# Kernel optimization log

Measured on AMD Instinct MI355X. Metric: run time of the kernel, lower is better.

## Reference

```python
import jax, jax.numpy as jnp
import numpy as np

BS, SEQ_LEN, N_NODES = 16, 12, 512
D, H, L, K = 256, 8, 2, 16
DFF = 4 * D
DH = D // H


def setup_inputs() -> dict:
    key = jax.random.key(0)
    ks = jax.random.split(key, 12)
    p = lambda i, shape: jax.random.normal(ks[i], shape, dtype=jnp.float32) * 0.02
    return dict(
        x_c=jax.random.normal(ks[0], (BS, SEQ_LEN, N_NODES), dtype=jnp.float32),
        A=jax.random.uniform(ks[1], (N_NODES, N_NODES), dtype=jnp.float32),
        W_src_emb=p(2, (SEQ_LEN, D)),
        W_tgt_emb=p(3, (SEQ_LEN, D)),
        enc_attn=p(4, (L, 4, D, D)),
        enc_ffn1=p(5, (L, D, DFF)),
        enc_ffn2=p(6, (L, DFF, D)),
        dec_self=p(7, (L, 4, D, D)),
        dec_cross=p(8, (L, 4, D, D)),
        dec_ffn1=p(9, (L, D, DFF)),
        dec_ffn2=p(10, (L, DFF, D)),
        W_gen=p(11, (D, SEQ_LEN)),
    )


def _ln(x):
    m = jnp.mean(x, axis=-1, keepdims=True)
    v = jnp.var(x, axis=-1, keepdims=True)
    return (x - m) * jax.lax.rsqrt(v + 1e-6)


def _mha(xq, xkv, W):
    # xq: [b, n, q, D], xkv: [b, n, s, D], W: [4, D, D]
    q = (xq @ W[0]).reshape(xq.shape[:-1] + (H, DH))
    k = (xkv @ W[1]).reshape(xkv.shape[:-1] + (H, DH))
    v = (xkv @ W[2]).reshape(xkv.shape[:-1] + (H, DH))
    sc = jnp.einsum('bnqhe,bnkhe->bnhqk', q, k) / np.float32(np.sqrt(DH))
    a = jax.nn.softmax(sc, axis=-1)
    o = jnp.einsum('bnhqk,bnkhe->bnqhe', a, v)
    o = o.reshape(o.shape[:-2] + (D,))
    return o @ W[3]


def _pe(length):
    pos = jnp.arange(length, dtype=jnp.float32)[:, None]
    div = jnp.exp(jnp.arange(0, D, 2, dtype=jnp.float32) * (-np.log(10000.0) / D))
    pe = jnp.zeros((length, D), dtype=jnp.float32)
    pe = pe.at[:, 0::2].set(jnp.sin(pos * div)).at[:, 1::2].set(jnp.cos(pos * div))
    return pe


def reference(x_c, A, W_src_emb, W_tgt_emb, enc_attn, enc_ffn1, enc_ffn2,
              dec_self, dec_cross, dec_ffn1, dec_ffn2, W_gen):
    # x_c: [bs, seq_len, N] -> x: [bs, N, seq_len]
    x = jnp.transpose(x_c, (0, 2, 1))
    # top-k neighbors per node (descending by A)
    index = jnp.argsort(-A, axis=-1)[:, :K]            # [N, K]
    sx = x[:, index]                                   # [bs, N, K, seq_len]  (the gather)
    tgt_in = x[:, :, None, :]                          # [bs, N, 1, seq_len]

    scale = np.float32(np.sqrt(D))
    src = sx @ W_src_emb * scale + _pe(K)              # [bs, N, K, D]
    tgt = tgt_in @ W_tgt_emb * scale + _pe(1)          # [bs, N, 1, D]

    # encoder (pre-norm residual sublayers, annotated-transformer style)
    for l in range(L):
        y = _ln(src)
        src = src + _mha(y, y, enc_attn[l])
        y = _ln(src)
        src = src + jax.nn.relu(y @ enc_ffn1[l]) @ enc_ffn2[l]
    memory = _ln(src)

    # decoder
    for l in range(L):
        y = _ln(tgt)
        tgt = tgt + _mha(y, y, dec_self[l])
        y = _ln(tgt)
        tgt = tgt + _mha(y, memory, dec_cross[l])
        y = _ln(tgt)
        tgt = tgt + jax.nn.relu(y @ dec_ffn1[l]) @ dec_ffn2[l]
    out = _ln(tgt) @ W_gen                             # [bs, N, 1, seq_len]
    return out[:, :, 0, :]                             # squeeze(-2): [bs, N, seq_len]
```

## Files before the change

kernel.cpp:

```cpp
#include <hip/hip_runtime.h>

typedef unsigned short u16;
typedef unsigned int u32;
typedef __attribute__((ext_vector_type(8))) short short8;
typedef __attribute__((ext_vector_type(4))) float f32x4;

__device__ __forceinline__ float bf2f(unsigned v){ union{unsigned u; float f;} c; c.u = v<<16; return c.f; }
__device__ __forceinline__ u16 f2bf(float f){
  union{float f; unsigned u;} c; c.f=f;
  unsigned u = c.u;
  u += 0x7fffu + ((u>>16)&1u);
  return (u16)(u>>16);
}
__device__ __forceinline__ float bfLO(u32 x){ union{u32 u; float f;} c; c.u = x<<16;        return c.f; }
__device__ __forceinline__ float bfHI(u32 x){ union{u32 u; float f;} c; c.u = x&0xffff0000u; return c.f; }
__device__ __forceinline__ u32 pack2(float a, float b){ return (u32)f2bf(a) | ((u32)f2bf(b)<<16); }

__device__ __forceinline__ float hsum32(float v){
  #pragma unroll
  for(int off=16; off>0; off>>=1) v += __shfl_xor(v, off);
  return v;
}

#define GLDS(g, l) __builtin_amdgcn_global_load_lds( \
    (const __attribute__((address_space(1))) void*)(g), \
    (__attribute__((address_space(3))) void*)(l), 16, 0, 0)

__global__ void topk_kernel(const float* __restrict__ A, int* __restrict__ idx){
  __shared__ float vals[512];
  const int n = blockIdx.x, t = threadIdx.x;
  for(int i=t;i<512;i+=64) vals[i] = A[n*512+i];
  __syncthreads();
  for(int kk=0;kk<16;kk++){
    float bv = -1e30f; int bi = 1<<30;
    for(int i=t;i<512;i+=64){
      float v = vals[i];
      if(v > bv){ bv=v; bi=i; }
    }
    #pragma unroll
    for(int off=32; off>0; off>>=1){
      float ov = __shfl_down(bv, off);
      int   oi = __shfl_down(bi, off);
      if(ov > bv || (ov==bv && oi<bi)){ bv=ov; bi=oi; }
    }
    bi = __shfl(bi, 0);
    if(t==0){ idx[n*16+kk] = bi; vals[bi] = -1e30f; }
    __syncthreads();
  }
}

__global__ __launch_bounds__(256)
void tcvt_kernel(const float* __restrict__ src, u16* __restrict__ dst, int R, int C){
  __shared__ float t[32][33];
  const int m = blockIdx.z;
  src += (size_t)m*R*C; dst += (size_t)m*R*C;
  const int c0 = blockIdx.x*32, r0 = blockIdx.y*32;
  const int tx = threadIdx.x, ty = threadIdx.y;
  #pragma unroll
  for(int i=0;i<4;i++) t[ty*4+i][tx] = src[(size_t)(r0+ty*4+i)*C + c0+tx];
  __syncthreads();
  #pragma unroll
  for(int i=0;i<4;i++) dst[(size_t)(c0+ty*4+i)*R + r0+tx] = f2bf(t[tx][ty*4+i]);
}

__global__ void cvt_kernel(const float* __restrict__ in, u16* __restrict__ out, int n4){
  int i = blockIdx.x*256 + threadIdx.x;
  if(i>=n4) return;
  float4 v = ((const float4*)in)[i];
  ushort4 o; o.x=f2bf(v.x); o.y=f2bf(v.y); o.z=f2bf(v.z); o.w=f2bf(v.w);
  ((ushort4*)out)[i] = o;
}

__global__ void embed_kernel(const float* __restrict__ x_c, const int* __restrict__ idx,
                             const float* __restrict__ Wsrc, const float* __restrict__ Wtgt,
                             u16* __restrict__ S, u16* __restrict__ TGT, int g0){
  __shared__ float xs[16][12];
  __shared__ float xt[12];
  const int gl = blockIdx.x, g = gl + g0, b = g>>9, n = g&511, d = threadIdx.x;
  if(d < 192){ int kk=d/12, t=d-kk*12; xs[kk][t] = x_c[(b*12+t)*512 + idx[n*16+kk]]; }
  else if(d < 204){ int t=d-192; xt[t] = x_c[(b*12+t)*512 + n]; }
  __syncthreads();
  float wsr[12], wtg[12];
  #pragma unroll
  for(int t=0;t<12;t++){ wsr[t]=Wsrc[t*256+d]; wtg[t]=Wtgt[t*256+d]; }
  const float freq = expf(-(float)(d & ~1) * (9.210340371976184f/256.0f));
  const bool odd = d & 1;
  for(int kk=0;kk<16;kk++){
    float a=0;
    #pragma unroll
    for(int t=0;t<12;t++) a = fmaf(xs[kk][t], wsr[t], a);
    float pe = odd ? cosf(freq*(float)kk) : sinf(freq*(float)kk);
    S[(size_t)(gl*16+kk)*256 + d] = f2bf(a*16.0f + pe);
  }
  float a=0;
  #pragma unroll
  for(int t=0;t<12;t++) a = fmaf(xt[t], wtg[t], a);
  TGT[(size_t)gl*256 + d] = f2bf(a*16.0f + (odd?1.0f:0.0f));
}

__global__ __launch_bounds__(256) void ln_kernel(const u16* __restrict__ X, u16* __restrict__ Y){
  const int tid = threadIdx.x;
  const int lh = tid & 31;
  const size_t row = (size_t)blockIdx.x*8 + (tid>>5);
  const size_t base = row*256 + (size_t)lh*8;
  uint4 u = *(const uint4*)(X + base);
  float x[8];
  x[0]=bfLO(u.x); x[1]=bfHI(u.x); x[2]=bfLO(u.y); x[3]=bfHI(u.y);
  x[4]=bfLO(u.z); x[5]=bfHI(u.z); x[6]=bfLO(u.w); x[7]=bfHI(u.w);
  float s=0;
  #pragma unroll
  for(int i=0;i<8;i++) s += x[i];
  float mean = hsum32(s) * (1.0f/256.0f);
  float v=0;
  #pragma unroll
  for(int i=0;i<8;i++){ x[i]-=mean; v += x[i]*x[i]; }
  float sc = rsqrtf(hsum32(v)*(1.0f/256.0f) + 1e-6f);
  uint4 o;
  o.x = pack2(x[0]*sc, x[1]*sc); o.y = pack2(x[2]*sc, x[3]*sc);
  o.z = pack2(x[4]*sc, x[5]*sc); o.w = pack2(x[6]*sc, x[7]*sc);
  *(uint4*)(Y + base) = o;
}

template<int MODE>
__global__ __launch_bounds__(256)
void gemm_mfma(const u16* __restrict__ A, const u16* __restrict__ Bt, u16* __restrict__ C,
               int M, int N, int K)
{
  __shared__ u16 As[128*32];
  __shared__ u16 Bs[128*32];
  const int tid = threadIdx.x;
  const int w = tid>>6, l = tid&63;
  const int quad = l>>4, col16 = l&15;
  const int wr = (w>>1)*64, wc = (w&1)*64;
  const size_t m0 = (size_t)blockIdx.x*128;
  const size_t n0 = (size_t)blockIdx.y*128;

  const int sr = l>>2, sc = (l&3)*8;
  const int ca = w*2, cb = w*2+1;
  const u16* aG0 = A  + (m0 + ca*16 + sr)*K + sc;
  const u16* aG1 = A  + (m0 + cb*16 + sr)*K + sc;
  const u16* bG0 = Bt + (n0 + ca*16 + sr)*K + sc;
  const u16* bG1 = Bt + (n0 + cb*16 + sr)*K + sc;
  u16* aL0 = &As[ca*512];
  u16* aL1 = &As[cb*512];
  u16* bL0 = &Bs[ca*512];
  u16* bL1 = &Bs[cb*512];

  f32x4 acc[4][4];
  #pragma unroll
  for(int i=0;i<4;i++)
    #pragma unroll
    for(int j=0;j<4;j++) acc[i][j] = (f32x4){0.f,0.f,0.f,0.f};

  for(int k0=0;k0<K;k0+=32){
    GLDS(aG0 + k0, aL0);
    GLDS(aG1 + k0, aL1);
    GLDS(bG0 + k0, bL0);
    GLDS(bG1 + k0, bL1);
    __syncthreads();
    short8 af[4], bf[4];
    #pragma unroll
    for(int i=0;i<4;i++) af[i] = *(const short8*)&As[(wr + i*16 + col16)*32 + quad*8];
    #pragma unroll
    for(int j=0;j<4;j++) bf[j] = *(const short8*)&Bs[(wc + j*16 + col16)*32 + quad*8];
    #pragma unroll
    for(int i=0;i<4;i++)
      #pragma unroll
      for(int j=0;j<4;j++)
        acc[i][j] = __builtin_amdgcn_mfma_f32_16x16x32_bf16(af[i], bf[j], acc[i][j], 0,0,0);
    __syncthreads();
  }

  #pragma unroll
  for(int i=0;i<4;i++){
    #pragma unroll
    for(int r=0;r<4;r++){
      const size_t row = m0 + wr + i*16 + quad*4 + r;
      u16* cp = C + row*(size_t)N + n0 + wc + col16;
      #pragma unroll
      for(int j=0;j<4;j++){
        float v = acc[i][j][r];
        if(MODE==2) v += bf2f(cp[j*16]);
        if(MODE==1) v = fmaxf(v, 0.f);
        cp[j*16] = f2bf(v);
      }
    }
  }
}

__global__ __launch_bounds__(256)
void attn_enc_kernel(const u16* __restrict__ QKV, u16* __restrict__ O){
  __shared__ u16 sh[2][12672];
  const int tid = threadIdx.x;
  const int half = tid>>7, th = tid&127;
  const size_t g = (size_t)blockIdx.x*2 + half;
  const size_t grow = g*16;
  u16* sb = sh[half];
  #pragma unroll
  for(int it=0; it<12; it++){
    int e = (th + 128*it)*8;
    int r = e/768, c = e - r*768;
    int t = c>>8, cc = c&255;
    *(uint4*)&sb[t*4224 + r*264 + cc] = *(const uint4*)&QKV[(grow+r)*768 + c];
  }
  __syncthreads();
  const int h = th>>4, q = th&15;
  const int ho = h*32;
  float qv[32];
  #pragma unroll
  for(int e2=0;e2<16;e2++){
    u32 x = *(const u32*)&sb[q*264 + ho + e2*2];
    qv[2*e2]=bfLO(x); qv[2*e2+1]=bfHI(x);
  }
  float sc[16];
  #pragma unroll
  for(int kk=0;kk<16;kk++){
    const u16* kr = &sb[4224 + kk*264 + ho];
    float s=0;
    #pragma unroll
    for(int e2=0;e2<16;e2++){
      u32 x = *(const u32*)&kr[e2*2];
      s = fmaf(qv[2*e2], bfLO(x), s);
      s = fmaf(qv[2*e2+1], bfHI(x), s);
    }
    sc[kk] = s*0.17677669529663687f;
  }
  float m=sc[0];
  #pragma unroll
  for(int kk=1;kk<16;kk++) m=fmaxf(m,sc[kk]);
  float sum=0;
  #pragma unroll
  for(int kk=0;kk<16;kk++){ sc[kk]=expf(sc[kk]-m); sum+=sc[kk]; }
  float inv=1.0f/sum;
  float ov[32];
  #pragma unroll
  for(int e=0;e<32;e++) ov[e]=0.f;
  #pragma unroll
  for(int kk=0;kk<16;kk++){
    float p = sc[kk]*inv;
    const u16* vr = &sb[8448 + kk*264 + ho];
    #pragma unroll
    for(int e2=0;e2<16;e2++){
      u32 x = *(const u32*)&vr[e2*2];
      ov[2*e2]   = fmaf(p, bfLO(x), ov[2*e2]);
      ov[2*e2+1] = fmaf(p, bfHI(x), ov[2*e2+1]);
    }
  }
  u16* op = O + (grow+q)*256 + ho;
  #pragma unroll
  for(int b=0;b<8;b++){
    ushort4 t4; t4.x=f2bf(ov[4*b]); t4.y=f2bf(ov[4*b+1]); t4.z=f2bf(ov[4*b+2]); t4.w=f2bf(ov[4*b+3]);
    *(ushort4*)&op[b*4] = t4;
  }
}

__global__ __launch_bounds__(256)
void attn_cross_kernel(const u16* __restrict__ Qc, const u16* __restrict__ KV,
                       u16* __restrict__ Oc, int loff){
  __shared__ float qs[256];
  __shared__ float ks[16*264], vs[16*264];
  __shared__ float aw[128];
  const int t = threadIdx.x;
  const size_t g = blockIdx.x;
  qs[t] = bf2f(Qc[g*256+t]);
  for(int i=t;i<4096;i+=256){
    int r=i>>8, c=i&255;
    int li = r*264 + ((c>>5)*33) + (c&31);
    const u16* p = KV + (g*16+r)*1024 + loff + c;
    ks[li]=bf2f(p[0]); vs[li]=bf2f(p[256]);
  }
  __syncthreads();
  if(t<128){
    int h=t>>4, kk=t&15;
    float s=0;
    #pragma unroll
    for(int e=0;e<32;e++) s = fmaf(qs[h*32+e], ks[kk*264+h*33+e], s);
    aw[h*16+kk] = s*0.17677669529663687f;
  }
  __syncthreads();
  if(t<8){
    float m=-1e30f;
    for(int kk=0;kk<16;kk++) m=fmaxf(m, aw[t*16+kk]);
    float sum=0;
    for(int kk=0;kk<16;kk++){ float e=expf(aw[t*16+kk]-m); aw[t*16+kk]=e; sum+=e; }
    float inv=1.0f/sum;
    for(int kk=0;kk<16;kk++) aw[t*16+kk]*=inv;
  }
  __syncthreads();
  {
    int h=t>>5, e=t&31;
    float o=0;
    #pragma unroll
    for(int kk=0;kk<16;kk++) o = fmaf(aw[h*16+kk], vs[kk*264+h*33+e], o);
    Oc[g*256+t] = f2bf(o);
  }
}

__global__ __launch_bounds__(64)
void final_kernel(const u16* __restrict__ T, const float* __restrict__ Wg, float* __restrict__ out, int g0){
  __shared__ float y[256];
  const int lane = threadIdx.x;
  const size_t gl = blockIdx.x;
  ushort4 u = *(const ushort4*)(T + gl*256 + (size_t)lane*4);
  float x0=bf2f(u.x), x1=bf2f(u.y), x2=bf2f(u.z), x3=bf2f(u.w);
  float s4 = x0+x1+x2+x3;
  #pragma unroll
  for(int off=32; off>0; off>>=1) s4 += __shfl_xor(s4, off);
  float mean = s4*(1.0f/256.0f);
  float d0=x0-mean,d1=x1-mean,d2=x2-mean,d3=x3-mean;
  float v4 = d0*d0+d1*d1+d2*d2+d3*d3;
  #pragma unroll
  for(int off=32; off>0; off>>=1) v4 += __shfl_xor(v4, off);
  float sc = rsqrtf(v4*(1.0f/256.0f)+1e-6f);
  y[lane*4+0]=d0*sc; y[lane*4+1]=d1*sc; y[lane*4+2]=d2*sc; y[lane*4+3]=d3*sc;
  __syncthreads();
  if(lane<12){
    float s=0;
    for(int d=0;d<256;d++) s = fmaf(y[d], Wg[d*12+lane], s);
    out[(g0+gl)*12+lane]=s;
  }
}

extern "C" void kernel_launch(void* const* d_in, const int* in_sizes, int n_in,
                              void* d_out, int out_size, void* d_ws, size_t ws_size,
                              hipStream_t stream)
{
  (void)in_sizes; (void)n_in; (void)out_size;
  const float* x_c  = (const float*)d_in[0];
  const float* A    = (const float*)d_in[1];
  const float* Wsrc = (const float*)d_in[2];
  const float* Wtgt = (const float*)d_in[3];
  const float* wsrc_f[7] = {(const float*)d_in[4],(const float*)d_in[5],(const float*)d_in[6],
                            (const float*)d_in[7],(const float*)d_in[8],(const float*)d_in[9],
                            (const float*)d_in[10]};
  const float* W_gen = (const float*)d_in[11];
  float* out = (float*)d_out;

  auto align256 = [](size_t b)->size_t{ return (b + 255) & ~(size_t)255; };
  auto need_bytes = [&](int GC)->size_t{
    size_t b = 0;
    b += align256(512*16*4);
    for(int i=0;i<7;i++) b += align256((size_t)524288*2);
    b += align256((size_t)4*65536*2);
    b += align256((size_t)2*65536*2)*2;
    b += align256((size_t)GC*16*256*2)*2;
    b += align256((size_t)GC*16*1024*2);
    b += align256((size_t)GC*256*2)*4;
    b += align256((size_t)GC*1024*2);
    return b;
  };
  int GC = 8192;
  while(GC > 128 && need_bytes(GC) > ws_size) GC >>= 1;

  char* ws = (char*)d_ws;
  size_t off = 0;
  auto alloc = [&](size_t bytes)->char*{
    char* p = ws + off;
    off += (bytes + 255) & ~(size_t)255;
    return p;
  };
  int* idx = (int*)alloc(512*16*4);
  u16* wt[7];
  for(int i=0;i<7;i++) wt[i] = (u16*)alloc((size_t)524288*2);
  u16* wKV      = (u16*)alloc((size_t)4*65536*2);
  u16* wv_plain = (u16*)alloc((size_t)2*65536*2);
  u16* wVO      = (u16*)alloc((size_t)2*65536*2);
  u16* cS  = (u16*)alloc((size_t)GC*16*256*2);
  u16* cY  = (u16*)alloc((size_t)GC*16*256*2);
  u16* big = (u16*)alloc((size_t)GC*16*1024*2);
  u16* tgt = (u16*)alloc((size_t)GC*256*2);
  u16* tY  = (u16*)alloc((size_t)GC*256*2);
  u16* tA  = (u16*)alloc((size_t)GC*256*2);
  u16* tO  = (u16*)alloc((size_t)GC*256*2);
  u16* tT  = (u16*)alloc((size_t)GC*1024*2);

  u16* wQKV = big;
  u16* Tc   = big;
  u16* KVc  = big;

  {
    dim3 blk(32,8);
    tcvt_kernel<<<dim3( 256/32, 256/32, 8), blk, 0, stream>>>(wsrc_f[0], wt[0], 256, 256);
    tcvt_kernel<<<dim3(1024/32, 256/32, 2), blk, 0, stream>>>(wsrc_f[1], wt[1], 256,1024);
    tcvt_kernel<<<dim3( 256/32,1024/32, 2), blk, 0, stream>>>(wsrc_f[2], wt[2],1024, 256);
    tcvt_kernel<<<dim3( 256/32, 256/32, 8), blk, 0, stream>>>(wsrc_f[3], wt[3], 256, 256);
    tcvt_kernel<<<dim3( 256/32, 256/32, 8), blk, 0, stream>>>(wsrc_f[4], wt[4], 256, 256);
    tcvt_kernel<<<dim3(1024/32, 256/32, 2), blk, 0, stream>>>(wsrc_f[5], wt[5], 256,1024);
    tcvt_kernel<<<dim3( 256/32,1024/32, 2), blk, 0, stream>>>(wsrc_f[6], wt[6],1024, 256);
  }
  topk_kernel<<<512,64,0,stream>>>(A, idx);

  hipMemcpyAsync(wKV+0*65536, wt[4]+1*65536, 65536*2, hipMemcpyDeviceToDevice, stream);
  hipMemcpyAsync(wKV+1*65536, wt[4]+2*65536, 65536*2, hipMemcpyDeviceToDevice, stream);
  hipMemcpyAsync(wKV+2*65536, wt[4]+5*65536, 65536*2, hipMemcpyDeviceToDevice, stream);
  hipMemcpyAsync(wKV+3*65536, wt[4]+6*65536, 65536*2, hipMemcpyDeviceToDevice, stream);

  for(int l=0;l<2;l++){
    cvt_kernel<<<64,256,0,stream>>>(wsrc_f[3]+(size_t)(l*4+2)*65536, wv_plain+(size_t)l*65536, 16384);
    gemm_mfma<0><<<dim3(2,2),256,0,stream>>>(wt[3]+(size_t)(l*4+3)*65536, wv_plain+(size_t)l*65536,
                                             wVO+(size_t)l*65536, 256,256,256);
  }

  auto gemm = [&](const u16* Am, const u16* Bm, u16* Cm, int M_, int N_, int K_, int mode){
    dim3 grid(M_/128, N_/128);
    if(mode==1)      gemm_mfma<1><<<grid,256,0,stream>>>(Am,Bm,Cm,M_,N_,K_);
    else if(mode==2) gemm_mfma<2><<<grid,256,0,stream>>>(Am,Bm,Cm,M_,N_,K_);
    else             gemm_mfma<0><<<grid,256,0,stream>>>(Am,Bm,Cm,M_,N_,K_);
  };

  const int Mr = GC*16;
  const int Md = GC;

  for(int g0=0; g0<8192; g0+=GC){
    embed_kernel<<<GC,256,0,stream>>>(x_c, idx, Wsrc, Wtgt, cS, tgt, g0);

    for(int l=0;l<2;l++){
      const u16* Wat = wt[0] + (size_t)l*4*65536;
      ln_kernel<<<Mr/8,256,0,stream>>>(cS, cY);
      gemm(cY, Wat,           wQKV, Mr, 768, 256, 0);
      attn_enc_kernel<<<GC/2,256,0,stream>>>(wQKV, cY);
      gemm(cY, Wat+3*65536,   cS,   Mr, 256, 256, 2);
      ln_kernel<<<Mr/8,256,0,stream>>>(cS, cY);
      gemm(cY, wt[1]+(size_t)l*262144, Tc, Mr,1024, 256, 1);
      gemm(Tc, wt[2]+(size_t)l*262144, cS, Mr, 256,1024, 2);
    }
    ln_kernel<<<Mr/8,256,0,stream>>>(cS, cY);
    gemm(cY, wKV, KVc, Mr, 1024, 256, 0);

    for(int l=0;l<2;l++){
      const u16* Wdc = wt[4] + (size_t)l*4*65536;
      ln_kernel<<<Md/8,256,0,stream>>>(tgt, tY);
      gemm(tY, wVO+(size_t)l*65536, tgt, Md, 256, 256, 2);
      ln_kernel<<<Md/8,256,0,stream>>>(tgt, tY);
      gemm(tY, Wdc,          tA,  Md, 256, 256, 0);
      attn_cross_kernel<<<GC,256,0,stream>>>(tA, KVc, tO, l*512);
      gemm(tO, Wdc+3*65536,  tgt, Md, 256, 256, 2);
      ln_kernel<<<Md/8,256,0,stream>>>(tgt, tY);
      gemm(tY, wt[5]+(size_t)l*262144, tT,  Md,1024, 256, 1);
      gemm(tT, wt[6]+(size_t)l*262144, tgt, Md, 256,1024, 2);
    }

    final_kernel<<<GC,64,0,stream>>>(tgt, W_gen, out, g0);
  }
}
```

Baseline: 1.902 ms.

## Fuse LayerNorm into residual GEMM epilogues and embedding kernel

Adds a gemm_addln kernel where each block covers a full 256-wide row, does the residual add, computes the row mean and variance across waves through shared memory, and writes both the residual stream and its normalized copy. The embedding kernel also emits the normalized source and target, and final_kernel now reads the already-normalized target. Together these remove every standalone ln_kernel launch and the extra read and write of activations it caused. In exchange the fused GEMM uses a 128x256 tile with a larger accumulator array, so register pressure rises and fewer blocks launch, and variance is now computed as E[x²]-mean², which is less numerically robust.

```diff
diff --git a/kernel.cpp b/kernel.cpp
--- a/kernel.cpp
+++ b/kernel.cpp
@@ -15,12 +15,6 @@
 __device__ __forceinline__ float bfLO(u32 x){ union{u32 u; float f;} c; c.u = x<<16;        return c.f; }
 __device__ __forceinline__ float bfHI(u32 x){ union{u32 u; float f;} c; c.u = x&0xffff0000u; return c.f; }
 __device__ __forceinline__ u32 pack2(float a, float b){ return (u32)f2bf(a) | ((u32)f2bf(b)<<16); }
-
-__device__ __forceinline__ float hsum32(float v){
-  #pragma unroll
-  for(int off=16; off>0; off>>=1) v += __shfl_xor(v, off);
-  return v;
-}
 
 #define GLDS(g, l) __builtin_amdgcn_global_load_lds( \
     (const __attribute__((address_space(1))) void*)(g), \
@@ -71,12 +65,19 @@
   ((ushort4*)out)[i] = o;
 }
 
-__global__ void embed_kernel(const float* __restrict__ x_c, const int* __restrict__ idx,
-                             const float* __restrict__ Wsrc, const float* __restrict__ Wtgt,
-                             u16* __restrict__ S, u16* __restrict__ TGT, int g0){
+__global__ __launch_bounds__(256)
+void embed_kernel(const float* __restrict__ x_c, const int* __restrict__ idx,
+                  const float* __restrict__ Wsrc, const float* __restrict__ Wtgt,
+                  u16* __restrict__ S, u16* __restrict__ SY,
+                  u16* __restrict__ TGT, u16* __restrict__ TGTY, int g0){
   __shared__ float xs[16][12];
   __shared__ float xt[12];
+  __shared__ float sm[16][260];
+  __shared__ float mv[16][2];
+  __shared__ float wpart[4][2];
+  __shared__ float tmv[2];
   const int gl = blockIdx.x, g = gl + g0, b = g>>9, n = g&511, d = threadIdx.x;
+  const int w = d>>6, lane = d&63;
   if(d < 192){ int kk=d/12, t=d-kk*12; xs[kk][t] = x_c[(b*12+t)*512 + idx[n*16+kk]]; }
   else if(d < 204){ int t=d-192; xt[t] = x_c[(b*12+t)*512 + n]; }
   __syncthreads();
@@ -85,40 +86,57 @@
   for(int t=0;t<12;t++){ wsr[t]=Wsrc[t*256+d]; wtg[t]=Wtgt[t*256+d]; }
   const float freq = expf(-(float)(d & ~1) * (9.210340371976184f/256.0f));
   const bool odd = d & 1;
+  float xv[16];
+  #pragma unroll
   for(int kk=0;kk<16;kk++){
     float a=0;
     #pragma unroll
     for(int t=0;t<12;t++) a = fmaf(xs[kk][t], wsr[t], a);
     float pe = odd ? cosf(freq*(float)kk) : sinf(freq*(float)kk);
-    S[(size_t)(gl*16+kk)*256 + d] = f2bf(a*16.0f + pe);
-  }
-  float a=0;
-  #pragma unroll
-  for(int t=0;t<12;t++) a = fmaf(xt[t], wtg[t], a);
-  TGT[(size_t)gl*256 + d] = f2bf(a*16.0f + (odd?1.0f:0.0f));
-}
-
-__global__ __launch_bounds__(256) void ln_kernel(const u16* __restrict__ X, u16* __restrict__ Y){
-  const int tid = threadIdx.x;
-  const int lh = tid & 31;
-  const size_t row = (size_t)blockIdx.x*8 + (tid>>5);
-  const size_t base = row*256 + (size_t)lh*8;
-  uint4 u = *(const uint4*)(X + base);
-  float x[8];
-  x[0]=bfLO(u.x); x[1]=bfHI(u.x); x[2]=bfLO(u.y); x[3]=bfHI(u.y);
-  x[4]=bfLO(u.z); x[5]=bfHI(u.z); x[6]=bfLO(u.w); x[7]=bfHI(u.w);
-  float s=0;
-  #pragma unroll
-  for(int i=0;i<8;i++) s += x[i];
-  float mean = hsum32(s) * (1.0f/256.0f);
-  float v=0;
-  #pragma unroll
-  for(int i=0;i<8;i++){ x[i]-=mean; v += x[i]*x[i]; }
-  float sc = rsqrtf(hsum32(v)*(1.0f/256.0f) + 1e-6f);
-  uint4 o;
-  o.x = pack2(x[0]*sc, x[1]*sc); o.y = pack2(x[2]*sc, x[3]*sc);
-  o.z = pack2(x[4]*sc, x[5]*sc); o.w = pack2(x[6]*sc, x[7]*sc);
-  *(uint4*)(Y + base) = o;
+    xv[kk] = a*16.0f + pe;
+    S[(size_t)(gl*16+kk)*256 + d] = f2bf(xv[kk]);
+    sm[kk][d] = xv[kk];
+  }
+  float tv;
+  {
+    float a=0;
+    #pragma unroll
+    for(int t=0;t<12;t++) a = fmaf(xt[t], wtg[t], a);
+    tv = a*16.0f + (odd?1.0f:0.0f);
+    TGT[(size_t)gl*256 + d] = f2bf(tv);
+  }
+  {
+    float s2=tv, q2=tv*tv;
+    #pragma unroll
+    for(int off=32; off>0; off>>=1){ s2+=__shfl_xor(s2,off); q2+=__shfl_xor(q2,off); }
+    if(lane==0){ wpart[w][0]=s2; wpart[w][1]=q2; }
+  }
+  __syncthreads();
+  {
+    const int kk=d>>4, part=d&15;
+    float s=0,q=0;
+    #pragma unroll
+    for(int t=0;t<16;t++){ float v=sm[kk][part*16+t]; s+=v; q+=v*v; }
+    #pragma unroll
+    for(int off=1; off<16; off<<=1){ s+=__shfl_xor(s,off); q+=__shfl_xor(q,off); }
+    if(part==0){
+      float mean=s*(1.0f/256.0f);
+      float var=q*(1.0f/256.0f)-mean*mean;
+      mv[kk][0]=mean; mv[kk][1]=rsqrtf(var+1e-6f);
+    }
+    if(d==0){
+      float ts=wpart[0][0]+wpart[1][0]+wpart[2][0]+wpart[3][0];
+      float tq=wpart[0][1]+wpart[1][1]+wpart[2][1]+wpart[3][1];
+      float mean=ts*(1.0f/256.0f);
+      float var=tq*(1.0f/256.0f)-mean*mean;
+      tmv[0]=mean; tmv[1]=rsqrtf(var+1e-6f);
+    }
+  }
+  __syncthreads();
+  #pragma unroll
+  for(int kk=0;kk<16;kk++)
+    SY[(size_t)(gl*16+kk)*256 + d] = f2bf((xv[kk]-mv[kk][0])*mv[kk][1]);
+  TGTY[(size_t)gl*256 + d] = f2bf((tv-tmv[0])*tmv[1]);
 }
 
 template<int MODE>
@@ -183,6 +201,98 @@
         if(MODE==2) v += bf2f(cp[j*16]);
         if(MODE==1) v = fmaxf(v, 0.f);
         cp[j*16] = f2bf(v);
+      }
+    }
+  }
+}
+
+__global__ __launch_bounds__(256,2)
+void gemm_addln(const u16* __restrict__ A, const u16* __restrict__ Bt,
+                u16* __restrict__ C, u16* __restrict__ Y, int M, int K)
+{
+  __shared__ u16 As[128*32];
+  __shared__ u16 Bs[256*32];
+  __shared__ float ssum[128][2];
+  __shared__ float ssq[128][2];
+  const int tid = threadIdx.x;
+  const int w = tid>>6, l = tid&63;
+  const int quad = l>>4, col16 = l&15;
+  const int wr = (w>>1)*64, wc = (w&1)*128;
+  const int wh = w&1;
+  const size_t m0 = (size_t)blockIdx.x*128;
+
+  const int sr = l>>2, sc = (l&3)*8;
+  const u16* aG0 = A + (m0 + (w*2+0)*16 + sr)*K + sc;
+  const u16* aG1 = A + (m0 + (w*2+1)*16 + sr)*K + sc;
+  u16* aL0 = &As[(w*2+0)*512];
+  u16* aL1 = &As[(w*2+1)*512];
+  const u16* bG[4]; u16* bL[4];
+  #pragma unroll
+  for(int c=0;c<4;c++){
+    int ch = w*4+c;
+    bG[c] = Bt + (size_t)(ch*16 + sr)*K + sc;
+    bL[c] = &Bs[ch*512];
+  }
+
+  f32x4 acc[4][8];
+  #pragma unroll
+  for(int i=0;i<4;i++)
+    #pragma unroll
+    for(int j=0;j<8;j++) acc[i][j] = (f32x4){0.f,0.f,0.f,0.f};
+
+  for(int k0=0;k0<K;k0+=32){
+    GLDS(aG0 + k0, aL0);
+    GLDS(aG1 + k0, aL1);
+    #pragma unroll
+    for(int c=0;c<4;c++) GLDS(bG[c] + k0, bL[c]);
+    __syncthreads();
+    short8 af[4], bf[8];
+    #pragma unroll
+    for(int i=0;i<4;i++) af[i] = *(const short8*)&As[(wr + i*16 + col16)*32 + quad*8];
+    #pragma unroll
+    for(int j=0;j<8;j++) bf[j] = *(const short8*)&Bs[(wc + j*16 + col16)*32 + quad*8];
+    #pragma unroll
+    for(int i=0;i<4;i++)
+      #pragma unroll
+      for(int j=0;j<8;j++)
+        acc[i][j] = __builtin_amdgcn_mfma_f32_16x16x32_bf16(af[i], bf[j], acc[i][j], 0,0,0);
+    __syncthreads();
+  }
+
+  #pragma unroll
+  for(int i=0;i<4;i++){
+    #pragma unroll
+    for(int r=0;r<4;r++){
+      const int lr = wr + i*16 + quad*4 + r;
+      const u16* cp = C + (m0 + lr)*(size_t)256 + wc + col16;
+      float s=0.f, q=0.f;
+      #pragma unroll
+      for(int j=0;j<8;j++){
+        float v = acc[i][j][r] + bf2f(cp[j*16]);
+        acc[i][j][r] = v;
+        s += v; q += v*v;
+      }
+      #pragma unroll
+      for(int off=1; off<16; off<<=1){ s+=__shfl_xor(s,off); q+=__shfl_xor(q,off); }
+      if(col16==0){ ssum[lr][wh]=s; ssq[lr][wh]=q; }
+    }
+  }
+  __syncthreads();
+  #pragma unroll
+  for(int i=0;i<4;i++){
+    #pragma unroll
+    for(int r=0;r<4;r++){
+      const int lr = wr + i*16 + quad*4 + r;
+      const float mean = (ssum[lr][0]+ssum[lr][1])*(1.0f/256.0f);
+      const float var  = (ssq[lr][0]+ssq[lr][1])*(1.0f/256.0f) - mean*mean;
+      const float rs   = rsqrtf(var + 1e-6f);
+      u16* cp = C + (m0 + lr)*(size_t)256 + wc + col16;
+      u16* yp = Y + (m0 + lr)*(size_t)256 + wc + col16;
+      #pragma unroll
+      for(int j=0;j<8;j++){
+        float v = acc[i][j][r];
+        cp[j*16] = f2bf(v);
+        yp[j*16] = f2bf((v-mean)*rs);
       }
     }
   }
@@ -297,22 +407,12 @@
 }
 
 __global__ __launch_bounds__(64)
-void final_kernel(const u16* __restrict__ T, const float* __restrict__ Wg, float* __restrict__ out, int g0){
+void final_kernel(const u16* __restrict__ TY, const float* __restrict__ Wg, float* __restrict__ out, int g0){
   __shared__ float y[256];
   const int lane = threadIdx.x;
   const size_t gl = blockIdx.x;
-  ushort4 u = *(const ushort4*)(T + gl*256 + (size_t)lane*4);
-  float x0=bf2f(u.x), x1=bf2f(u.y), x2=bf2f(u.z), x3=bf2f(u.w);
-  float s4 = x0+x1+x2+x3;
-  #pragma unroll
-  for(int off=32; off>0; off>>=1) s4 += __shfl_xor(s4, off);
-  float mean = s4*(1.0f/256.0f);
-  float d0=x0-mean,d1=x1-mean,d2=x2-mean,d3=x3-mean;
-  float v4 = d0*d0+d1*d1+d2*d2+d3*d3;
-  #pragma unroll
-  for(int off=32; off>0; off>>=1) v4 += __shfl_xor(v4, off);
-  float sc = rsqrtf(v4*(1.0f/256.0f)+1e-6f);
-  y[lane*4+0]=d0*sc; y[lane*4+1]=d1*sc; y[lane*4+2]=d2*sc; y[lane*4+3]=d3*sc;
+  ushort4 u = *(const ushort4*)(TY + gl*256 + (size_t)lane*4);
+  y[lane*4+0]=bf2f(u.x); y[lane*4+1]=bf2f(u.y); y[lane*4+2]=bf2f(u.z); y[lane*4+3]=bf2f(u.w);
   __syncthreads();
   if(lane<12){
     float s=0;
@@ -407,39 +507,36 @@
     else if(mode==2) gemm_mfma<2><<<grid,256,0,stream>>>(Am,Bm,Cm,M_,N_,K_);
     else             gemm_mfma<0><<<grid,256,0,stream>>>(Am,Bm,Cm,M_,N_,K_);
   };
+  auto gemm_ln = [&](const u16* Am, const u16* Bm, u16* Cm, u16* Ym, int M_, int K_){
+    gemm_addln<<<dim3(M_/128),256,0,stream>>>(Am,Bm,Cm,Ym,M_,K_);
+  };
 
   const int Mr = GC*16;
   const int Md = GC;
 
   for(int g0=0; g0<8192; g0+=GC){
-    embed_kernel<<<GC,256,0,stream>>>(x_c, idx, Wsrc, Wtgt, cS, tgt, g0);
+    embed_kernel<<<GC,256,0,stream>>>(x_c, idx, Wsrc, Wtgt, cS, cY, tgt, tY, g0);
 
     for(int l=0;l<2;l++){
       const u16* Wat = wt[0] + (size_t)l*4*65536;
-      ln_kernel<<<Mr/8,256,0,stream>>>(cS, cY);
-      gemm(cY, Wat,           wQKV, Mr, 768, 256, 0);
+      gemm(cY, Wat, wQKV, Mr, 768, 256, 0);
       attn_enc_kernel<<<GC/2,256,0,stream>>>(wQKV, cY);
-      gemm(cY, Wat+3*65536,   cS,   Mr, 256, 256, 2);
-      ln_kernel<<<Mr/8,256,0,stream>>>(cS, cY);
+      gemm_ln(cY, Wat+3*65536, cS, cY, Mr, 256);
       gemm(cY, wt[1]+(size_t)l*262144, Tc, Mr,1024, 256, 1);
-      gemm(Tc, wt[2]+(size_t)l*262144, cS, Mr, 256,1024, 2);
-    }
-    ln_kernel<<<Mr/8,256,0,stream>>>(cS, cY);
+      gemm_ln(Tc, wt[2]+(size_t)l*262144, cS, cY, Mr, 1024);
+    }
     gemm(cY, wKV, KVc, Mr, 1024, 256, 0);
 
     for(int l=0;l<2;l++){
       const u16* Wdc = wt[4] + (size_t)l*4*65536;
-      ln_kernel<<<Md/8,256,0,stream>>>(tgt, tY);
-      gemm(tY, wVO+(size_t)l*65536, tgt, Md, 256, 256, 2);
-      ln_kernel<<<Md/8,256,0,stream>>>(tgt, tY);
-      gemm(tY, Wdc,          tA,  Md, 256, 256, 0);
+      gemm_ln(tY, wVO+(size_t)l*65536, tgt, tY, Md, 256);
+      gemm(tY, Wdc, tA, Md, 256, 256, 0);
       attn_cross_kernel<<<GC,256,0,stream>>>(tA, KVc, tO, l*512);
-      gemm(tO, Wdc+3*65536,  tgt, Md, 256, 256, 2);
-      ln_kernel<<<Md/8,256,0,stream>>>(tgt, tY);
-      gemm(tY, wt[5]+(size_t)l*262144, tT,  Md,1024, 256, 1);
-      gemm(tT, wt[6]+(size_t)l*262144, tgt, Md, 256,1024, 2);
-    }
-
-    final_kernel<<<GC,64,0,stream>>>(tgt, W_gen, out, g0);
-  }
-}
+      gemm_ln(tO, Wdc+3*65536, tgt, tY, Md, 256);
+      gemm(tY, wt[5]+(size_t)l*262144, tT, Md,1024, 256, 1);
+      gemm_ln(tT, wt[6]+(size_t)l*262144, tgt, tY, Md, 1024);
+    }
+
+    final_kernel<<<GC,64,0,stream>>>(tY, W_gen, out, g0);
+  }
+}
```

New measurement: 1.857 ms. 1.02x faster.
